# Kernel tuning notes

Hardware: AMD Instinct MI355X
Metric: run time of the kernel (lower is better)

Reference implementation:

```python
import jax, jax.numpy as jnp
import numpy as np

N = 6144
IN_DIM = 256
HID = 64
HEADS = 4
LAT = 32
ALPHA = 0.2  # LeakyReLU negative slope
NEG_INF = -9e15


def setup_inputs() -> dict:
    key = jax.random.key(0)
    ks = jax.random.split(key, 6)
    x = jax.random.normal(ks[0], (N, IN_DIM), jnp.float32)
    # sparse symmetric 0/1 adjacency, avg degree ~ 25
    A = (jax.random.uniform(ks[1], (N, N)) < 0.004).astype(jnp.float32)
    A = jnp.maximum(A, A.T)
    # xavier-uniform-ish params, matching pyGAT GraphAttentionLayer shapes
    s1 = float(np.sqrt(6.0 / (IN_DIM + HID)))
    W_heads = jax.random.uniform(ks[2], (HEADS, IN_DIM, HID), jnp.float32, -s1, s1)
    sa = float(np.sqrt(6.0 / (2 * HID + 1)))
    a_heads = jax.random.uniform(ks[3], (HEADS, 2 * HID), jnp.float32, -sa, sa)
    s2 = float(np.sqrt(6.0 / (HEADS * HID + LAT)))
    W_out = jax.random.uniform(ks[4], (HEADS * HID, LAT), jnp.float32, -s2, s2)
    sb = float(np.sqrt(6.0 / (2 * LAT + 1)))
    a_out = jax.random.uniform(ks[5], (2 * LAT,), jnp.float32, -sb, sb)
    return {"x": x, "A": A, "W_heads": W_heads, "a_heads": a_heads,
            "W_out": W_out, "a_out": a_out}


def _gat_layer(h, adj_mask, W, a, concat):
    # h: [N, F_in], W: [F_in, F], a: [2F]
    Wh = h @ W                              # [N, F]
    f = W.shape[1]
    e_src = Wh @ a[:f]                      # [N]
    e_dst = Wh @ a[f:]                      # [N]
    e = jax.nn.leaky_relu(e_src[:, None] + e_dst[None, :], ALPHA)  # [N, N]
    e = jnp.where(adj_mask, e, NEG_INF)
    att = jax.nn.softmax(e, axis=1)         # masked softmax over neighbors
    out = att @ Wh                          # [N, F]
    return jax.nn.elu(out) if concat else out


def reference(x, A, W_heads, a_heads, W_out, a_out):
    # normalize(A, 'sym', False): D^{-1/2} A D^{-1/2}
    deg = A.sum(axis=1)
    dinv = jnp.where(deg > 0, deg ** -0.5, 0.0)
    An = A * dinv[:, None] * dinv[None, :]
    mask = An > 0
    heads = [_gat_layer(x, mask, W_heads[i], a_heads[i], True) for i in range(HEADS)]
    h = jnp.concatenate(heads, axis=1)      # [N, HEADS*HID]
    z = jax.nn.elu(_gat_layer(h, mask, W_out, a_out, False))  # [N, LAT]
    return jax.nn.sigmoid(z @ z.T)          # [N, N]
```

## Files before the change

### kernel.cpp

```cpp
#include <hip/hip_runtime.h>
#include <hip/hip_bf16.h>

#define NN 6144
#define IN_DIM 256
#define HID 64
#define HEADS 4
#define LAT 32
#define CAP 192
#define ALPHA 0.2f
#define GEMM_BLOCKS 384

__device__ __forceinline__ float elu_f(float v)   { return v > 0.f ? v : expm1f(v); }
__device__ __forceinline__ float lrelu_f(float v) { return v > 0.f ? v : ALPHA * v; }

__global__ __launch_bounds__(256) void k_pre(const float* __restrict__ A,
                                             const float* __restrict__ x,
                                             const float* __restrict__ Wheads,
                                             const float* __restrict__ aheads,
                                             int* __restrict__ nbr, int* __restrict__ cnt,
                                             float* __restrict__ Wh,
                                             float* __restrict__ es, float* __restrict__ ed) {
    __shared__ __align__(16) float smem[2048];
    int bid = blockIdx.x;
    int t = threadIdx.x;
    if (bid < GEMM_BLOCKS) {
        int head = bid & 3, m0 = (bid >> 2) * 64;
        float (*As)[64] = (float(*)[64])smem;
        float (*Bs)[64] = (float(*)[64])(smem + 1024);
        const float* Wc = Wheads + (size_t)head * IN_DIM * HID;
        int ty = t >> 4, tx = t & 15;
        float acc[4][4] = {};
        for (int k0 = 0; k0 < IN_DIM; k0 += 16) {
            {
                int row = t >> 2, k4 = (t & 3) * 4;
                float4 v = *(const float4*)(x + (size_t)(m0 + row) * IN_DIM + k0 + k4);
                As[k4 + 0][row] = v.x; As[k4 + 1][row] = v.y;
                As[k4 + 2][row] = v.z; As[k4 + 3][row] = v.w;
                int kk = t >> 4, n4 = (t & 15) * 4;
                *(float4*)&Bs[kk][n4] = *(const float4*)(Wc + (size_t)(k0 + kk) * HID + n4);
            }
            __syncthreads();
            #pragma unroll
            for (int k = 0; k < 16; ++k) {
                float4 av = *(float4*)&As[k][ty * 4];
                float4 bv = *(float4*)&Bs[k][tx * 4];
                float ar[4] = {av.x, av.y, av.z, av.w};
                float br[4] = {bv.x, bv.y, bv.z, bv.w};
                #pragma unroll
                for (int i = 0; i < 4; ++i)
                    #pragma unroll
                    for (int j = 0; j < 4; ++j)
                        acc[i][j] = fmaf(ar[i], br[j], acc[i][j]);
            }
            __syncthreads();
        }
        #pragma unroll
        for (int i = 0; i < 4; ++i) {
            float4 o = make_float4(acc[i][0], acc[i][1], acc[i][2], acc[i][3]);
            *(float4*)(Wh + (size_t)(m0 + ty * 4 + i) * (HEADS * HID) + head * HID + tx * 4) = o;
        }
        float4 a1v = *(const float4*)(aheads + head * 2 * HID + tx * 4);
        float4 a2v = *(const float4*)(aheads + head * 2 * HID + HID + tx * 4);
        #pragma unroll
        for (int i = 0; i < 4; ++i) {
            float p1 = acc[i][0] * a1v.x + acc[i][1] * a1v.y + acc[i][2] * a1v.z + acc[i][3] * a1v.w;
            float p2 = acc[i][0] * a2v.x + acc[i][1] * a2v.y + acc[i][2] * a2v.z + acc[i][3] * a2v.w;
            #pragma unroll
            for (int off = 8; off; off >>= 1) {
                p1 += __shfl_down(p1, off, 16);
                p2 += __shfl_down(p2, off, 16);
            }
            if (tx == 0) {
                es[head * NN + m0 + ty * 4 + i] = p1;
                ed[head * NN + m0 + ty * 4 + i] = p2;
            }
        }
    } else {
        int row = bid - GEMM_BLOCKS;
        int* lcnt = (int*)smem;
        const float4* Arow = (const float4*)(A + (size_t)row * NN);
        if (t == 0) *lcnt = 0;
        __syncthreads();
        int* my = nbr + (size_t)row * CAP;
        #pragma unroll
        for (int it = 0; it < NN / 4 / 256; ++it) {
            int idx4 = it * 256 + t;
            float4 v = Arow[idx4];
            int base = idx4 * 4;
            if (v.x != 0.f) { int p = atomicAdd(lcnt, 1); if (p < CAP) my[p] = base; }
            if (v.y != 0.f) { int p = atomicAdd(lcnt, 1); if (p < CAP) my[p] = base + 1; }
            if (v.z != 0.f) { int p = atomicAdd(lcnt, 1); if (p < CAP) my[p] = base + 2; }
            if (v.w != 0.f) { int p = atomicAdd(lcnt, 1); if (p < CAP) my[p] = base + 3; }
        }
        __syncthreads();
        if (t == 0) cnt[row] = *lcnt < CAP ? *lcnt : CAP;
    }
}

__global__ __launch_bounds__(256) void k_attn1g2(const int* __restrict__ nbr, const int* __restrict__ cnt,
                                                 const float* __restrict__ es, const float* __restrict__ ed,
                                                 const float* __restrict__ Wh,
                                                 const float* __restrict__ Wout, const float* __restrict__ aout,
                                                 float* __restrict__ Wh2,
                                                 float* __restrict__ es2, float* __restrict__ ed2) {
    __shared__ int col[CAP];
    __shared__ float att[HEADS][CAP];
    __shared__ float hrow[HEADS * HID];
    __shared__ float part[8][LAT];
    int i = blockIdx.x;
    int t = threadIdx.x, h = t >> 6, l = t & 63;
    int c = cnt[i];
    float hval;
    if (c == 0) {
        float s = 0.f;
        for (int r = 0; r < NN; ++r) s += Wh[(size_t)r * (HEADS * HID) + h * HID + l];
        hval = elu_f(s * (1.0f / NN));
    } else {
        const int* nb = nbr + (size_t)i * CAP;
        float esi = es[h * NN + i];
        float m = -3.0e38f;
        for (int j = l; j < c; j += 64) {
            int cj = nb[j];
            if (h == 0) col[j] = cj;
            float e = lrelu_f(esi + ed[h * NN + cj]);
            att[h][j] = e;
            m = fmaxf(m, e);
        }
        #pragma unroll
        for (int off = 32; off; off >>= 1) m = fmaxf(m, __shfl_down(m, off));
        m = __shfl(m, 0);
        float s = 0.f;
        for (int j = l; j < c; j += 64) {
            float p = __expf(att[h][j] - m);
            att[h][j] = p;
            s += p;
        }
        #pragma unroll
        for (int off = 32; off; off >>= 1) s += __shfl_down(s, off);
        s = __shfl(s, 0);
        __syncthreads();
        float inv = 1.0f / s;
        const float* WhH = Wh + h * HID + l;
        float acc0 = 0.f, acc1 = 0.f, acc2 = 0.f, acc3 = 0.f;
        int j = 0;
        for (; j + 4 <= c; j += 4) {
            acc0 = fmaf(att[h][j + 0], WhH[(size_t)col[j + 0] * (HEADS * HID)], acc0);
            acc1 = fmaf(att[h][j + 1], WhH[(size_t)col[j + 1] * (HEADS * HID)], acc1);
            acc2 = fmaf(att[h][j + 2], WhH[(size_t)col[j + 2] * (HEADS * HID)], acc2);
            acc3 = fmaf(att[h][j + 3], WhH[(size_t)col[j + 3] * (HEADS * HID)], acc3);
        }
        for (; j < c; ++j)
            acc0 = fmaf(att[h][j], WhH[(size_t)col[j] * (HEADS * HID)], acc0);
        hval = elu_f(((acc0 + acc1) + (acc2 + acc3)) * inv);
    }
    hrow[h * HID + l] = hval;
    __syncthreads();
    {
        int half = l >> 5, cc = l & 31;
        int tbase = h * HID + half * 32;
        float p = 0.f;
        #pragma unroll 8
        for (int tt = 0; tt < 32; ++tt)
            p = fmaf(hrow[tbase + tt], Wout[(tbase + tt) * LAT + cc], p);
        part[h * 2 + half][cc] = p;
    }
    __syncthreads();
    if (t < 32) {
        float acc = 0.f;
        #pragma unroll
        for (int w = 0; w < 8; ++w) acc += part[w][t];
        Wh2[(size_t)i * LAT + t] = acc;
        float p1 = acc * aout[t], p2 = acc * aout[LAT + t];
        #pragma unroll
        for (int off = 16; off; off >>= 1) {
            p1 += __shfl_down(p1, off, 32);
            p2 += __shfl_down(p2, off, 32);
        }
        if (t == 0) { es2[i] = p1; ed2[i] = p2; }
    }
}

__global__ __launch_bounds__(256) void k_attn2(const int* __restrict__ nbr, const int* __restrict__ cnt,
                                               const float* __restrict__ es2, const float* __restrict__ ed2,
                                               const float* __restrict__ Wh2,
                                               float* __restrict__ z) {
    __shared__ float att[4][CAP];
    __shared__ int col[4][CAP];
    int w = threadIdx.x >> 6, l = threadIdx.x & 63;
    int i = blockIdx.x * 4 + w;
    int c = cnt[i];
    if (c == 0) {
        if (l < LAT) {
            float s = 0.f;
            for (int r = 0; r < NN; ++r) s += Wh2[(size_t)r * LAT + l];
            z[(size_t)i * LAT + l] = elu_f(s * (1.0f / NN));
        }
        return;
    }
    float esi = es2[i];
    const int* nb = nbr + (size_t)i * CAP;
    float m = -3.0e38f;
    for (int j = l; j < c; j += 64) {
        int cj = nb[j];
        col[w][j] = cj;
        float e = lrelu_f(esi + ed2[cj]);
        att[w][j] = e;
        m = fmaxf(m, e);
    }
    #pragma unroll
    for (int off = 32; off; off >>= 1) m = fmaxf(m, __shfl_down(m, off));
    m = __shfl(m, 0);
    float s = 0.f;
    for (int j = l; j < c; j += 64) {
        float p = __expf(att[w][j] - m);
        att[w][j] = p;
        s += p;
    }
    #pragma unroll
    for (int off = 32; off; off >>= 1) s += __shfl_down(s, off);
    s = __shfl(s, 0);
    if (l < LAT) {
        float inv = 1.0f / s;
        float acc0 = 0.f, acc1 = 0.f, acc2 = 0.f, acc3 = 0.f;
        int j = 0;
        for (; j + 4 <= c; j += 4) {
            acc0 = fmaf(att[w][j + 0], Wh2[(size_t)col[w][j + 0] * LAT + l], acc0);
            acc1 = fmaf(att[w][j + 1], Wh2[(size_t)col[w][j + 1] * LAT + l], acc1);
            acc2 = fmaf(att[w][j + 2], Wh2[(size_t)col[w][j + 2] * LAT + l], acc2);
            acc3 = fmaf(att[w][j + 3], Wh2[(size_t)col[w][j + 3] * LAT + l], acc3);
        }
        for (; j < c; ++j)
            acc0 = fmaf(att[w][j], Wh2[(size_t)col[w][j] * LAT + l], acc0);
        z[(size_t)i * LAT + l] = elu_f(((acc0 + acc1) + (acc2 + acc3)) * inv);
    }
}

__global__ __launch_bounds__(256) void k_zzt(const float* __restrict__ z, float* __restrict__ out) {
    __shared__ float zr[LAT][128];
    __shared__ float zc[LAT][128];
    int m0 = blockIdx.y * 128, n0 = blockIdx.x * 128;
    int t = threadIdx.x;
    #pragma unroll
    for (int it = 0; it < 4; ++it) {
        int chunk = it * 256 + t;
        int row = chunk >> 3, k4 = (chunk & 7) * 4;
        float4 v = *(const float4*)(z + (size_t)(m0 + row) * LAT + k4);
        zr[k4 + 0][row] = v.x; zr[k4 + 1][row] = v.y; zr[k4 + 2][row] = v.z; zr[k4 + 3][row] = v.w;
        float4 u = *(const float4*)(z + (size_t)(n0 + row) * LAT + k4);
        zc[k4 + 0][row] = u.x; zc[k4 + 1][row] = u.y; zc[k4 + 2][row] = u.z; zc[k4 + 3][row] = u.w;
    }
    __syncthreads();
    int ty = t >> 4, tx = t & 15;
    float acc[2][2][4][4] = {};
    #pragma unroll 4
    for (int k = 0; k < LAT; ++k) {
        float4 a0 = *(float4*)&zr[k][ty * 4];
        float4 a1 = *(float4*)&zr[k][64 + ty * 4];
        float4 b0 = *(float4*)&zc[k][tx * 4];
        float4 b1 = *(float4*)&zc[k][64 + tx * 4];
        float ar[2][4] = {{a0.x, a0.y, a0.z, a0.w}, {a1.x, a1.y, a1.z, a1.w}};
        float br[2][4] = {{b0.x, b0.y, b0.z, b0.w}, {b1.x, b1.y, b1.z, b1.w}};
        #pragma unroll
        for (int p = 0; p < 2; ++p)
            #pragma unroll
            for (int q = 0; q < 2; ++q)
                #pragma unroll
                for (int i = 0; i < 4; ++i)
                    #pragma unroll
                    for (int j = 0; j < 4; ++j)
                        acc[p][q][i][j] = fmaf(ar[p][i], br[q][j], acc[p][q][i][j]);
    }
    #pragma unroll
    for (int p = 0; p < 2; ++p) {
        #pragma unroll
        for (int i = 0; i < 4; ++i) {
            int row = m0 + p * 64 + ty * 4 + i;
            #pragma unroll
            for (int q = 0; q < 2; ++q) {
                float4 o;
                o.x = 1.0f / (1.0f + __expf(-acc[p][q][i][0]));
                o.y = 1.0f / (1.0f + __expf(-acc[p][q][i][1]));
                o.z = 1.0f / (1.0f + __expf(-acc[p][q][i][2]));
                o.w = 1.0f / (1.0f + __expf(-acc[p][q][i][3]));
                *(float4*)(out + (size_t)row * NN + n0 + q * 64 + tx * 4) = o;
            }
        }
    }
}

extern "C" void kernel_launch(void* const* d_in, const int* in_sizes, int n_in,
                              void* d_out, int out_size, void* d_ws, size_t ws_size,
                              hipStream_t stream) {
    const float* x      = (const float*)d_in[0];
    const float* A      = (const float*)d_in[1];
    const float* Wheads = (const float*)d_in[2];
    const float* aheads = (const float*)d_in[3];
    const float* Wout   = (const float*)d_in[4];
    const float* aout   = (const float*)d_in[5];
    float* out = (float*)d_out;

    char* ws = (char*)d_ws;
    size_t o = 0;
    auto alloc = [&](size_t bytes) { void* p = ws + o; o += (bytes + 255) & ~(size_t)255; return p; };
    int*   nbr   = (int*)  alloc((size_t)NN * CAP * 4);
    int*   cnt   = (int*)  alloc((size_t)NN * 4);
    float* Wh    = (float*)alloc((size_t)NN * HEADS * HID * 4);
    float* es    = (float*)alloc((size_t)HEADS * NN * 4);
    float* ed    = (float*)alloc((size_t)HEADS * NN * 4);
    float* Wh2   = (float*)alloc((size_t)NN * LAT * 4);
    float* es2   = (float*)alloc((size_t)NN * 4);
    float* ed2   = (float*)alloc((size_t)NN * 4);
    float* zbuf  = (float*)alloc((size_t)NN * LAT * 4);

    k_pre     <<<GEMM_BLOCKS + NN, 256, 0, stream>>>(A, x, Wheads, aheads, nbr, cnt, Wh, es, ed);
    k_attn1g2 <<<NN, 256, 0, stream>>>(nbr, cnt, es, ed, Wh, Wout, aout, Wh2, es2, ed2);
    k_attn2   <<<NN / 4, 256, 0, stream>>>(nbr, cnt, es2, ed2, Wh2, zbuf);
    k_zzt     <<<dim3(NN / 128, NN / 128), 256, 0, stream>>>(zbuf, out);
}
```

Before: 127.1 us.

## Compute sigmoid(z z^T) with split-bf16 MFMA instead of FP32 FMA tiles

New measurement: 114.9 us. 9.6% less time.

```diff
diff --git a/kernel.cpp b/kernel.cpp
--- a/kernel.cpp
+++ b/kernel.cpp
@@ -10,8 +10,19 @@
 #define ALPHA 0.2f
 #define GEMM_BLOCKS 384
 
+typedef __attribute__((ext_vector_type(8))) short bf16x8;
+typedef __attribute__((ext_vector_type(4))) float f32x4;
+
 __device__ __forceinline__ float elu_f(float v)   { return v > 0.f ? v : expm1f(v); }
 __device__ __forceinline__ float lrelu_f(float v) { return v > 0.f ? v : ALPHA * v; }
+
+__device__ __forceinline__ void split_bf16(float v, unsigned short& hi, unsigned short& lo) {
+    unsigned u = __builtin_bit_cast(unsigned, v);
+    hi = (unsigned short)(u >> 16);
+    float vh = __builtin_bit_cast(float, u & 0xFFFF0000u);
+    float rl = v - vh;
+    lo = (unsigned short)(__builtin_bit_cast(unsigned, rl) >> 16);
+}
 
 __global__ __launch_bounds__(256) void k_pre(const float* __restrict__ A,
                                              const float* __restrict__ x,
@@ -183,7 +194,7 @@
 __global__ __launch_bounds__(256) void k_attn2(const int* __restrict__ nbr, const int* __restrict__ cnt,
                                                const float* __restrict__ es2, const float* __restrict__ ed2,
                                                const float* __restrict__ Wh2,
-                                               float* __restrict__ z) {
+                                               unsigned short* __restrict__ zh, unsigned short* __restrict__ zl) {
     __shared__ float att[4][CAP];
     __shared__ int col[4][CAP];
     int w = threadIdx.x >> 6, l = threadIdx.x & 63;
@@ -193,7 +204,10 @@
         if (l < LAT) {
             float s = 0.f;
             for (int r = 0; r < NN; ++r) s += Wh2[(size_t)r * LAT + l];
-            z[(size_t)i * LAT + l] = elu_f(s * (1.0f / NN));
+            unsigned short hi, lo;
+            split_bf16(elu_f(s * (1.0f / NN)), hi, lo);
+            zh[(size_t)i * LAT + l] = hi;
+            zl[(size_t)i * LAT + l] = lo;
         }
         return;
     }
@@ -231,59 +245,36 @@
         }
         for (; j < c; ++j)
             acc0 = fmaf(att[w][j], Wh2[(size_t)col[w][j] * LAT + l], acc0);
-        z[(size_t)i * LAT + l] = elu_f(((acc0 + acc1) + (acc2 + acc3)) * inv);
-    }
-}
-
-__global__ __launch_bounds__(256) void k_zzt(const float* __restrict__ z, float* __restrict__ out) {
-    __shared__ float zr[LAT][128];
-    __shared__ float zc[LAT][128];
-    int m0 = blockIdx.y * 128, n0 = blockIdx.x * 128;
-    int t = threadIdx.x;
+        unsigned short hi, lo;
+        split_bf16(elu_f(((acc0 + acc1) + (acc2 + acc3)) * inv), hi, lo);
+        zh[(size_t)i * LAT + l] = hi;
+        zl[(size_t)i * LAT + l] = lo;
+    }
+}
+
+__global__ __launch_bounds__(256) void k_zzt(const unsigned short* __restrict__ zh,
+                                             const unsigned short* __restrict__ zl,
+                                             float* __restrict__ out) {
+    int t = threadIdx.x, w = t >> 6, l = t & 63;
+    int m0 = blockIdx.y * 64 + w * 16;
+    int n0 = blockIdx.x * 64;
+    int r = l & 15, kg = (l >> 4) * 8;
+    bf16x8 ah = *(const bf16x8*)(zh + (size_t)(m0 + r) * LAT + kg);
+    bf16x8 al = *(const bf16x8*)(zl + (size_t)(m0 + r) * LAT + kg);
     #pragma unroll
-    for (int it = 0; it < 4; ++it) {
-        int chunk = it * 256 + t;
-        int row = chunk >> 3, k4 = (chunk & 7) * 4;
-        float4 v = *(const float4*)(z + (size_t)(m0 + row) * LAT + k4);
-        zr[k4 + 0][row] = v.x; zr[k4 + 1][row] = v.y; zr[k4 + 2][row] = v.z; zr[k4 + 3][row] = v.w;
-        float4 u = *(const float4*)(z + (size_t)(n0 + row) * LAT + k4);
-        zc[k4 + 0][row] = u.x; zc[k4 + 1][row] = u.y; zc[k4 + 2][row] = u.z; zc[k4 + 3][row] = u.w;
-    }
-    __syncthreads();
-    int ty = t >> 4, tx = t & 15;
-    float acc[2][2][4][4] = {};
-    #pragma unroll 4
-    for (int k = 0; k < LAT; ++k) {
-        float4 a0 = *(float4*)&zr[k][ty * 4];
-        float4 a1 = *(float4*)&zr[k][64 + ty * 4];
-        float4 b0 = *(float4*)&zc[k][tx * 4];
-        float4 b1 = *(float4*)&zc[k][64 + tx * 4];
-        float ar[2][4] = {{a0.x, a0.y, a0.z, a0.w}, {a1.x, a1.y, a1.z, a1.w}};
-        float br[2][4] = {{b0.x, b0.y, b0.z, b0.w}, {b1.x, b1.y, b1.z, b1.w}};
-        #pragma unroll
-        for (int p = 0; p < 2; ++p)
-            #pragma unroll
-            for (int q = 0; q < 2; ++q)
-                #pragma unroll
-                for (int i = 0; i < 4; ++i)
-                    #pragma unroll
-                    for (int j = 0; j < 4; ++j)
-                        acc[p][q][i][j] = fmaf(ar[p][i], br[q][j], acc[p][q][i][j]);
-    }
-    #pragma unroll
-    for (int p = 0; p < 2; ++p) {
-        #pragma unroll
-        for (int i = 0; i < 4; ++i) {
-            int row = m0 + p * 64 + ty * 4 + i;
-            #pragma unroll
-            for (int q = 0; q < 2; ++q) {
-                float4 o;
-                o.x = 1.0f / (1.0f + __expf(-acc[p][q][i][0]));
-                o.y = 1.0f / (1.0f + __expf(-acc[p][q][i][1]));
-                o.z = 1.0f / (1.0f + __expf(-acc[p][q][i][2]));
-                o.w = 1.0f / (1.0f + __expf(-acc[p][q][i][3]));
-                *(float4*)(out + (size_t)row * NN + n0 + q * 64 + tx * 4) = o;
-            }
+    for (int j = 0; j < 4; ++j) {
+        int nb = n0 + j * 16;
+        bf16x8 bh = *(const bf16x8*)(zh + (size_t)(nb + r) * LAT + kg);
+        bf16x8 bl = *(const bf16x8*)(zl + (size_t)(nb + r) * LAT + kg);
+        f32x4 acc = {0.f, 0.f, 0.f, 0.f};
+        acc = __builtin_amdgcn_mfma_f32_16x16x32_bf16(ah, bh, acc, 0, 0, 0);
+        acc = __builtin_amdgcn_mfma_f32_16x16x32_bf16(ah, bl, acc, 0, 0, 0);
+        acc = __builtin_amdgcn_mfma_f32_16x16x32_bf16(al, bh, acc, 0, 0, 0);
+        #pragma unroll
+        for (int rr = 0; rr < 4; ++rr) {
+            int row = m0 + (l >> 4) * 4 + rr;
+            int colo = nb + (l & 15);
+            out[(size_t)row * NN + colo] = 1.0f / (1.0f + __expf(-acc[rr]));
         }
     }
 }
@@ -310,10 +301,11 @@
     float* Wh2   = (float*)alloc((size_t)NN * LAT * 4);
     float* es2   = (float*)alloc((size_t)NN * 4);
     float* ed2   = (float*)alloc((size_t)NN * 4);
-    float* zbuf  = (float*)alloc((size_t)NN * LAT * 4);
+    unsigned short* zh = (unsigned short*)alloc((size_t)NN * LAT * 2);
+    unsigned short* zl = (unsigned short*)alloc((size_t)NN * LAT * 2);
 
     k_pre     <<<GEMM_BLOCKS + NN, 256, 0, stream>>>(A, x, Wheads, aheads, nbr, cnt, Wh, es, ed);
     k_attn1g2 <<<NN, 256, 0, stream>>>(nbr, cnt, es, ed, Wh, Wout, aout, Wh2, es2, ed2);
-    k_attn2   <<<NN / 4, 256, 0, stream>>>(nbr, cnt, es2, ed2, Wh2, zbuf);
-    k_zzt     <<<dim3(NN / 128, NN / 128), 256, 0, stream>>>(zbuf, out);
-}
+    k_attn2   <<<NN / 4, 256, 0, stream>>>(nbr, cnt, es2, ed2, Wh2, zh, zl);
+    k_zzt     <<<dim3(NN / 64, NN / 64), 256, 0, stream>>>(zh, zl, out);
+}
```
